# Kernel optimization log

Measured on AMD Instinct MI355X. Metric: run time of the kernel, lower is better.

Reference implementation:

```python
import jax, jax.numpy as jnp
import numpy as np

NUM_ITERATIONS = 3

def _squash(s):
    # Original squash reduces over the trailing singleton dim -> elementwise.
    sn = s * s
    return sn * s / ((1.0 + sn) * jnp.sqrt(sn))

def setup_inputs() -> dict:
    key = jax.random.key(0)
    k1, k2 = jax.random.split(key)
    x = jax.random.normal(k1, (128, 1152, 8), dtype=jnp.float32)
    W = jax.random.normal(k2, (1, 1152, 16, 16, 8), dtype=jnp.float32)
    return {"x": x, "W": W}

def reference(x, W):
    # x: [B, R, I]; W: [1, R, C, O, I]
    Wr = W[0]  # [R, C, O, I]
    # u_hat = W @ x broadcast over capsules: [B, R, C, O]
    u_hat = jnp.einsum('rcoi,bri->brco', Wr, x)
    R, C = Wr.shape[0], Wr.shape[1]
    b = jnp.zeros((R, C), dtype=x.dtype)  # routing logits (shared across batch)
    v = None
    for it in range(NUM_ITERATIONS):
        # legacy F.softmax on [1,R,C,1] -> dim=1 == routes axis
        c = jax.nn.softmax(b, axis=0)  # [R, C]
        s = jnp.einsum('rc,brco->bco', c, u_hat)  # [B, C, O]
        v = _squash(s)
        if it < NUM_ITERATIONS - 1:
            # agreement: <u_hat, v> averaged over batch
            a = jnp.einsum('brco,bco->brc', u_hat, v).mean(axis=0)  # [R, C]
            b = b + a
    return v  # [B, C, O] == v_j.squeeze(1).squeeze(-1)
```

## Files before the change

### kernel.cpp

```cpp
#include <hip/hip_runtime.h>
#include <math.h>

#define B_   128
#define R_   1152
#define C_   16
#define O_   16
#define RS_  64
#define RCH_ 18

#define WS_SP   0
#define WS_V    2097152
#define WS_BLOG 2129920
#define WS_WT   2148352

__device__ __forceinline__ float squashf(float s) {
    return s * fabsf(s) / (1.0f + s * s);
}

__global__ __launch_bounds__(512) void wtrans_k(const float* __restrict__ W,
                                                float* __restrict__ wt) {
    const int r = blockIdx.x;
    const int t = threadIdx.x;
    __shared__ float4 sh[520];
    const float4* __restrict__ W4 = (const float4*)W;
    float4* __restrict__ Wt4 = (float4*)wt;

    sh[(t & 7) * 65 + (t >> 3)] = W4[r * 512 + t];
    __syncthreads();
    Wt4[r * 512 + t] = sh[(t >> 6) * 65 + (t & 63)];
}

template <bool FIRST>
__global__ __launch_bounds__(256) void gemm_s_k(const float* __restrict__ x,
                                                const float* __restrict__ wt,
                                                const float* __restrict__ blog,
                                                float* __restrict__ sp) {
    const int bt  = blockIdx.x;
    const int rs  = blockIdx.y;
    const int t   = threadIdx.x;
    const int co4 = t & 63;
    const int b4  = t >> 6;
    const int c   = co4 >> 2;
    const int r0  = rs * RCH_;

    __shared__ float4 xl4[576];
    __shared__ float4 part[16];
    __shared__ float  colinv[16];
    __shared__ float  cwl[RCH_ * 16];

    const float4* __restrict__ X4  = (const float4*)x;
    const float4* __restrict__ Wt4 = (const float4*)wt;

    #pragma unroll
    for (int k = 0; k < 3; ++k) {
        const int u = t + k * 256;
        if (u < 576) {
            const int bl = u / 36, rem = u % 36;
            xl4[u] = X4[((bt * 16 + bl) * R_ + r0) * 2 + rem];
        }
    }

    if (!FIRST) {
        const float4* BL4 = (const float4*)blog;
        const int g = t & 3;
        float4 e4; e4.x = 0.f; e4.y = 0.f; e4.z = 0.f; e4.w = 0.f;
        #pragma unroll
        for (int i = 0; i < 18; ++i) {
            const float4 bv = BL4[i * 256 + t];
            e4.x += __expf(bv.x); e4.y += __expf(bv.y);
            e4.z += __expf(bv.z); e4.w += __expf(bv.w);
        }
        #pragma unroll
        for (int d = 4; d < 64; d <<= 1) {
            e4.x += __shfl_xor(e4.x, d); e4.y += __shfl_xor(e4.y, d);
            e4.z += __shfl_xor(e4.z, d); e4.w += __shfl_xor(e4.w, d);
        }
        if ((t & 63) < 4) part[(t >> 6) * 4 + g] = e4;
        __syncthreads();
        if (t < 4) {
            const float4 a = part[t], b = part[4 + t], cc4 = part[8 + t], d = part[12 + t];
            colinv[t * 4 + 0] = 1.0f / ((a.x + b.x) + (cc4.x + d.x));
            colinv[t * 4 + 1] = 1.0f / ((a.y + b.y) + (cc4.y + d.y));
            colinv[t * 4 + 2] = 1.0f / ((a.z + b.z) + (cc4.z + d.z));
            colinv[t * 4 + 3] = 1.0f / ((a.w + b.w) + (cc4.w + d.w));
        }
        __syncthreads();
        for (int u2 = t; u2 < RCH_ * 16; u2 += 256) {
            const int rl = u2 >> 4, cc = u2 & 15;
            cwl[u2] = __expf(blog[(r0 + rl) * 16 + cc]) * colinv[cc];
        }
    }
    __syncthreads();

    float acc[4][4];
    #pragma unroll
    for (int j = 0; j < 4; ++j)
        #pragma unroll
        for (int q = 0; q < 4; ++q) acc[j][q] = 0.f;

    #pragma unroll 3
    for (int rr = 0; rr < RCH_; ++rr) {
        const float cwv = FIRST ? (1.0f / (float)R_) : cwl[rr * 16 + c];
        const float4* wp = Wt4 + ((size_t)(r0 + rr) << 9) + co4;
        const float4 w0 = wp[  0], w1 = wp[ 64], w2 = wp[128], w3 = wp[192];
        const float4 w4 = wp[256], w5 = wp[320], w6 = wp[384], w7 = wp[448];
        #pragma unroll
        for (int j = 0; j < 4; ++j) {
            const float4 xa = xl4[(b4 * 4 + j) * 36 + rr * 2];
            const float4 xb = xl4[(b4 * 4 + j) * 36 + rr * 2 + 1];
            const float d0 = w0.x*xa.x + w0.y*xa.y + w0.z*xa.z + w0.w*xa.w
                           + w1.x*xb.x + w1.y*xb.y + w1.z*xb.z + w1.w*xb.w;
            const float d1 = w2.x*xa.x + w2.y*xa.y + w2.z*xa.z + w2.w*xa.w
                           + w3.x*xb.x + w3.y*xb.y + w3.z*xb.z + w3.w*xb.w;
            const float d2 = w4.x*xa.x + w4.y*xa.y + w4.z*xa.z + w4.w*xa.w
                           + w5.x*xb.x + w5.y*xb.y + w5.z*xb.z + w5.w*xb.w;
            const float d3 = w6.x*xa.x + w6.y*xa.y + w6.z*xa.z + w6.w*xa.w
                           + w7.x*xb.x + w7.y*xb.y + w7.z*xb.z + w7.w*xb.w;
            acc[j][0] = fmaf(cwv, d0, acc[j][0]);
            acc[j][1] = fmaf(cwv, d1, acc[j][1]);
            acc[j][2] = fmaf(cwv, d2, acc[j][2]);
            acc[j][3] = fmaf(cwv, d3, acc[j][3]);
        }
    }

    float4* sp4 = (float4*)sp;
    #pragma unroll
    for (int j = 0; j < 4; ++j) {
        const int b = bt * 16 + b4 * 4 + j;
        float4 o4; o4.x = acc[j][0]; o4.y = acc[j][1]; o4.z = acc[j][2]; o4.w = acc[j][3];
        sp4[(rs * B_ + b) * 64 + co4] = o4;
    }
}

__global__ __launch_bounds__(512) void reduce_squash_k(const float* __restrict__ sp,
                                                       float* __restrict__ outv) {
    const int t   = threadIdx.x;
    const int li  = t & 127;
    const int kq  = t >> 7;
    const int idx = blockIdx.x * 128 + li;
    const float* p = sp + (size_t)kq * 16 * 32768 + idx;
    float a0 = 0.f, a1 = 0.f, a2 = 0.f, a3 = 0.f;
    #pragma unroll
    for (int k = 0; k < 16; k += 4) {
        a0 += p[(k + 0) * 32768];
        a1 += p[(k + 1) * 32768];
        a2 += p[(k + 2) * 32768];
        a3 += p[(k + 3) * 32768];
    }
    __shared__ float red[512];
    red[t] = (a0 + a1) + (a2 + a3);
    __syncthreads();
    if (t < 128) {
        const float s = (red[t] + red[t + 128]) + (red[t + 256] + red[t + 384]);
        outv[idx] = squashf(s);
    }
}

template <bool FIRST>
__global__ __launch_bounds__(512) void a_k(const float* __restrict__ x,
                                           const float* __restrict__ wt,
                                           const float* __restrict__ v,
                                           float* __restrict__ blog) {
    const int r0 = blockIdx.x * 4;
    const int t  = threadIdx.x;
    const int w  = t >> 6, lane = t & 63;
    const int rr = w & 3, half = w >> 2;
    const int co4 = lane, c = lane >> 2;

    __shared__ float4 xl[128 * 8];
    __shared__ float  red[128];
    const float4* __restrict__ X4  = (const float4*)x;
    const float4* __restrict__ V4  = (const float4*)v;
    const float4* __restrict__ Wt4 = (const float4*)wt;

    #pragma unroll
    for (int kk = 0; kk < 2; ++kk) {
        const int u = t + kk * 512;
        const int b = u >> 3, rem = u & 7;
        xl[u] = X4[(b * R_ + r0) * 2 + rem];
    }
    __syncthreads();

    float y[8][4];
    #pragma unroll
    for (int i = 0; i < 8; ++i)
        #pragma unroll
        for (int q = 0; q < 4; ++q) y[i][q] = 0.f;

    const int b0 = half * 64;
    #pragma unroll 4
    for (int bb = 0; bb < 64; ++bb) {
        const int b = b0 + bb;
        const float4 xa = xl[b * 8 + rr * 2];
        const float4 xb = xl[b * 8 + rr * 2 + 1];
        const float4 vv = V4[b * 64 + co4];
        const float xs[8] = {xa.x, xa.y, xa.z, xa.w, xb.x, xb.y, xb.z, xb.w};
        #pragma unroll
        for (int i = 0; i < 8; ++i) {
            y[i][0] = fmaf(xs[i], vv.x, y[i][0]);
            y[i][1] = fmaf(xs[i], vv.y, y[i][1]);
            y[i][2] = fmaf(xs[i], vv.z, y[i][2]);
            y[i][3] = fmaf(xs[i], vv.w, y[i][3]);
        }
    }

    const float4* wp = Wt4 + ((size_t)(r0 + rr) << 9) + co4;
    float part = 0.f;
    #pragma unroll
    for (int q = 0; q < 4; ++q) {
        const float4 w0 = wp[(2 * q) * 64];
        const float4 w1 = wp[(2 * q + 1) * 64];
        part += w0.x*y[0][q] + w0.y*y[1][q] + w0.z*y[2][q] + w0.w*y[3][q]
              + w1.x*y[4][q] + w1.y*y[5][q] + w1.z*y[6][q] + w1.w*y[7][q];
    }
    part += __shfl_xor(part, 1);
    part += __shfl_xor(part, 2);
    if ((lane & 3) == 0) red[w * 16 + c] = part;
    __syncthreads();
    if (t < 64) {
        const int rr2 = t >> 4, cc = t & 15;
        const float val = (red[rr2 * 16 + cc] + red[(rr2 + 4) * 16 + cc]) * (1.0f / (float)B_);
        const int idx = (r0 + rr2) * 16 + cc;
        blog[idx] = FIRST ? val : (blog[idx] + val);
    }
}

extern "C" void kernel_launch(void* const* d_in, const int* in_sizes, int n_in,
                              void* d_out, int out_size, void* d_ws, size_t ws_size,
                              hipStream_t stream) {
    const float* x = (const float*)d_in[0];
    const float* W = (const float*)d_in[1];
    float* out = (float*)d_out;
    float* ws  = (float*)d_ws;

    float* sp   = ws + WS_SP;
    float* v    = ws + WS_V;
    float* blog = ws + WS_BLOG;
    float* wt   = ws + WS_WT;

    wtrans_k<<<R_, 512, 0, stream>>>(W, wt);

    gemm_s_k<true><<<dim3(8, RS_), 256, 0, stream>>>(x, wt, blog, sp);
    reduce_squash_k<<<256, 512, 0, stream>>>(sp, v);
    a_k<true><<<288, 512, 0, stream>>>(x, wt, v, blog);

    gemm_s_k<false><<<dim3(8, RS_), 256, 0, stream>>>(x, wt, blog, sp);
    reduce_squash_k<<<256, 512, 0, stream>>>(sp, v);
    a_k<false><<<288, 512, 0, stream>>>(x, wt, v, blog);

    gemm_s_k<false><<<dim3(8, RS_), 256, 0, stream>>>(x, wt, blog, sp);
    reduce_squash_k<<<256, 512, 0, stream>>>(sp, out);
}
```

Measured before the change: 179.3 us.

## Fuse reduce-squash into gemm via last-blocks finish, atomic softmax column sums

The separate reduce_squash kernel is removed. Each gemm block bumps an atomic counter, and the last 128 blocks spin until all blocks finish, then reduce the split-R partials and apply squash. The softmax column sums are now accumulated with atomics in the agreement kernel, so the gemm no longer recomputes them from the whole blog array. The kernel also adds register double-buffering of W loads, a block-index swizzle, and smaller agreement blocks. The spin-wait assumes all 512 blocks can be resident or finish, which risks a deadlock, and float atomics make the column sums nondeterministic.

Result: slower. 300.6 us (+67.7%).

```diff
diff --git a/kernel.cpp b/kernel.cpp
--- a/kernel.cpp
+++ b/kernel.cpp
@@ -7,24 +7,30 @@
 #define O_   16
 #define RS_  64
 #define RCH_ 18
+#define NBLK 512
+#define NFIN 128
 
 #define WS_SP   0
 #define WS_V    2097152
 #define WS_BLOG 2129920
-#define WS_WT   2148352
+#define WS_CTRL 2148352
+#define WS_WT   2148416
 
 __device__ __forceinline__ float squashf(float s) {
     return s * fabsf(s) / (1.0f + s * s);
 }
 
 __global__ __launch_bounds__(512) void wtrans_k(const float* __restrict__ W,
-                                                float* __restrict__ wt) {
+                                                float* __restrict__ wt,
+                                                float* __restrict__ ctrl) {
     const int r = blockIdx.x;
     const int t = threadIdx.x;
     __shared__ float4 sh[520];
     const float4* __restrict__ W4 = (const float4*)W;
     float4* __restrict__ Wt4 = (float4*)wt;
 
+    if (r == 0 && t < 64) ctrl[t] = 0.0f;
+
     sh[(t & 7) * 65 + (t >> 3)] = W4[r * 512 + t];
     __syncthreads();
     Wt4[r * 512 + t] = sh[(t >> 6) * 65 + (t & 63)];
@@ -34,9 +40,13 @@
 __global__ __launch_bounds__(256) void gemm_s_k(const float* __restrict__ x,
                                                 const float* __restrict__ wt,
                                                 const float* __restrict__ blog,
-                                                float* __restrict__ sp) {
-    const int bt  = blockIdx.x;
-    const int rs  = blockIdx.y;
+                                                const float* __restrict__ colsum,
+                                                float* __restrict__ sp,
+                                                float* __restrict__ dst,
+                                                unsigned int* __restrict__ ctr) {
+    const int bid = blockIdx.x;
+    const int bt  = bid >> 6;
+    const int rs  = ((bid & 7) << 3) | ((bid >> 3) & 7);
     const int t   = threadIdx.x;
     const int co4 = t & 63;
     const int b4  = t >> 6;
@@ -44,9 +54,10 @@
     const int r0  = rs * RCH_;
 
     __shared__ float4 xl4[576];
-    __shared__ float4 part[16];
-    __shared__ float  colinv[16];
     __shared__ float  cwl[RCH_ * 16];
+    __shared__ float  colinv_sh[16];
+    __shared__ float4 red[256];
+    __shared__ unsigned int old_sh;
 
     const float4* __restrict__ X4  = (const float4*)x;
     const float4* __restrict__ Wt4 = (const float4*)wt;
@@ -61,33 +72,11 @@
     }
 
     if (!FIRST) {
-        const float4* BL4 = (const float4*)blog;
-        const int g = t & 3;
-        float4 e4; e4.x = 0.f; e4.y = 0.f; e4.z = 0.f; e4.w = 0.f;
-        #pragma unroll
-        for (int i = 0; i < 18; ++i) {
-            const float4 bv = BL4[i * 256 + t];
-            e4.x += __expf(bv.x); e4.y += __expf(bv.y);
-            e4.z += __expf(bv.z); e4.w += __expf(bv.w);
-        }
-        #pragma unroll
-        for (int d = 4; d < 64; d <<= 1) {
-            e4.x += __shfl_xor(e4.x, d); e4.y += __shfl_xor(e4.y, d);
-            e4.z += __shfl_xor(e4.z, d); e4.w += __shfl_xor(e4.w, d);
-        }
-        if ((t & 63) < 4) part[(t >> 6) * 4 + g] = e4;
-        __syncthreads();
-        if (t < 4) {
-            const float4 a = part[t], b = part[4 + t], cc4 = part[8 + t], d = part[12 + t];
-            colinv[t * 4 + 0] = 1.0f / ((a.x + b.x) + (cc4.x + d.x));
-            colinv[t * 4 + 1] = 1.0f / ((a.y + b.y) + (cc4.y + d.y));
-            colinv[t * 4 + 2] = 1.0f / ((a.z + b.z) + (cc4.z + d.z));
-            colinv[t * 4 + 3] = 1.0f / ((a.w + b.w) + (cc4.w + d.w));
-        }
+        if (t < 16) colinv_sh[t] = 1.0f / colsum[t];
         __syncthreads();
         for (int u2 = t; u2 < RCH_ * 16; u2 += 256) {
             const int rl = u2 >> 4, cc = u2 & 15;
-            cwl[u2] = __expf(blog[(r0 + rl) * 16 + cc]) * colinv[cc];
+            cwl[u2] = __expf(blog[(r0 + rl) * 16 + cc]) * colinv_sh[cc];
         }
     }
     __syncthreads();
@@ -98,30 +87,43 @@
         #pragma unroll
         for (int q = 0; q < 4; ++q) acc[j][q] = 0.f;
 
-    #pragma unroll 3
-    for (int rr = 0; rr < RCH_; ++rr) {
+    const float4* __restrict__ wbase = Wt4 + ((size_t)r0 << 9) + co4;
+
+    auto body = [&](int rr, const float4* wv) {
         const float cwv = FIRST ? (1.0f / (float)R_) : cwl[rr * 16 + c];
-        const float4* wp = Wt4 + ((size_t)(r0 + rr) << 9) + co4;
-        const float4 w0 = wp[  0], w1 = wp[ 64], w2 = wp[128], w3 = wp[192];
-        const float4 w4 = wp[256], w5 = wp[320], w6 = wp[384], w7 = wp[448];
         #pragma unroll
         for (int j = 0; j < 4; ++j) {
             const float4 xa = xl4[(b4 * 4 + j) * 36 + rr * 2];
             const float4 xb = xl4[(b4 * 4 + j) * 36 + rr * 2 + 1];
-            const float d0 = w0.x*xa.x + w0.y*xa.y + w0.z*xa.z + w0.w*xa.w
-                           + w1.x*xb.x + w1.y*xb.y + w1.z*xb.z + w1.w*xb.w;
-            const float d1 = w2.x*xa.x + w2.y*xa.y + w2.z*xa.z + w2.w*xa.w
-                           + w3.x*xb.x + w3.y*xb.y + w3.z*xb.z + w3.w*xb.w;
-            const float d2 = w4.x*xa.x + w4.y*xa.y + w4.z*xa.z + w4.w*xa.w
-                           + w5.x*xb.x + w5.y*xb.y + w5.z*xb.z + w5.w*xb.w;
-            const float d3 = w6.x*xa.x + w6.y*xa.y + w6.z*xa.z + w6.w*xa.w
-                           + w7.x*xb.x + w7.y*xb.y + w7.z*xb.z + w7.w*xb.w;
+            const float d0 = wv[0].x*xa.x + wv[0].y*xa.y + wv[0].z*xa.z + wv[0].w*xa.w
+                           + wv[1].x*xb.x + wv[1].y*xb.y + wv[1].z*xb.z + wv[1].w*xb.w;
+            const float d1 = wv[2].x*xa.x + wv[2].y*xa.y + wv[2].z*xa.z + wv[2].w*xa.w
+                           + wv[3].x*xb.x + wv[3].y*xb.y + wv[3].z*xb.z + wv[3].w*xb.w;
+            const float d2 = wv[4].x*xa.x + wv[4].y*xa.y + wv[4].z*xa.z + wv[4].w*xa.w
+                           + wv[5].x*xb.x + wv[5].y*xb.y + wv[5].z*xb.z + wv[5].w*xb.w;
+            const float d3 = wv[6].x*xa.x + wv[6].y*xa.y + wv[6].z*xa.z + wv[6].w*xa.w
+                           + wv[7].x*xb.x + wv[7].y*xb.y + wv[7].z*xb.z + wv[7].w*xb.w;
             acc[j][0] = fmaf(cwv, d0, acc[j][0]);
             acc[j][1] = fmaf(cwv, d1, acc[j][1]);
             acc[j][2] = fmaf(cwv, d2, acc[j][2]);
             acc[j][3] = fmaf(cwv, d3, acc[j][3]);
         }
-    }
+    };
+
+    float4 w[8];
+    #pragma unroll
+    for (int q = 0; q < 8; ++q) w[q] = wbase[q * 64];
+    #pragma unroll 2
+    for (int rr = 0; rr < RCH_ - 1; ++rr) {
+        float4 wn[8];
+        const float4* wp = wbase + ((size_t)(rr + 1) << 9);
+        #pragma unroll
+        for (int q = 0; q < 8; ++q) wn[q] = wp[q * 64];
+        body(rr, w);
+        #pragma unroll
+        for (int q = 0; q < 8; ++q) w[q] = wn[q];
+    }
+    body(RCH_ - 1, w);
 
     float4* sp4 = (float4*)sp;
     #pragma unroll
@@ -130,53 +132,70 @@
         float4 o4; o4.x = acc[j][0]; o4.y = acc[j][1]; o4.z = acc[j][2]; o4.w = acc[j][3];
         sp4[(rs * B_ + b) * 64 + co4] = o4;
     }
-}
-
-__global__ __launch_bounds__(512) void reduce_squash_k(const float* __restrict__ sp,
-                                                       float* __restrict__ outv) {
-    const int t   = threadIdx.x;
-    const int li  = t & 127;
-    const int kq  = t >> 7;
-    const int idx = blockIdx.x * 128 + li;
-    const float* p = sp + (size_t)kq * 16 * 32768 + idx;
-    float a0 = 0.f, a1 = 0.f, a2 = 0.f, a3 = 0.f;
-    #pragma unroll
-    for (int k = 0; k < 16; k += 4) {
-        a0 += p[(k + 0) * 32768];
-        a1 += p[(k + 1) * 32768];
-        a2 += p[(k + 2) * 32768];
-        a3 += p[(k + 3) * 32768];
-    }
-    __shared__ float red[512];
-    red[t] = (a0 + a1) + (a2 + a3);
-    __syncthreads();
-    if (t < 128) {
-        const float s = (red[t] + red[t + 128]) + (red[t + 256] + red[t + 384]);
-        outv[idx] = squashf(s);
+
+    __syncthreads();
+    if (t == 0) {
+        __threadfence();
+        old_sh = atomicAdd(ctr, 1u);
+    }
+    __syncthreads();
+    const unsigned int old = old_sh;
+    if (old < (unsigned int)(NBLK - NFIN)) return;
+    const int fid = (int)old - (NBLK - NFIN);
+
+    if (t == 0) {
+        while (__hip_atomic_load(ctr, __ATOMIC_RELAXED, __HIP_MEMORY_SCOPE_AGENT)
+               < (unsigned int)NBLK) {
+            __builtin_amdgcn_s_sleep(2);
+        }
+    }
+    __syncthreads();
+    __threadfence();
+
+    const int li = t & 63, kq = t >> 6;
+    const int out4 = fid * 64 + li;
+    const float4* __restrict__ sp4c = (const float4*)sp;
+    float4 a; a.x = 0.f; a.y = 0.f; a.z = 0.f; a.w = 0.f;
+    #pragma unroll
+    for (int k = 0; k < 16; ++k) {
+        const float4 u = sp4c[(size_t)(kq * 16 + k) * 8192 + out4];
+        a.x += u.x; a.y += u.y; a.z += u.z; a.w += u.w;
+    }
+    red[t] = a;
+    __syncthreads();
+    if (t < 64) {
+        const float4 p0 = red[t], p1 = red[t + 64], p2 = red[t + 128], p3 = red[t + 192];
+        float4 o;
+        o.x = squashf((p0.x + p1.x) + (p2.x + p3.x));
+        o.y = squashf((p0.y + p1.y) + (p2.y + p3.y));
+        o.z = squashf((p0.z + p1.z) + (p2.z + p3.z));
+        o.w = squashf((p0.w + p1.w) + (p2.w + p3.w));
+        ((float4*)dst)[fid * 64 + t] = o;
     }
 }
 
 template <bool FIRST>
-__global__ __launch_bounds__(512) void a_k(const float* __restrict__ x,
+__global__ __launch_bounds__(256) void a_k(const float* __restrict__ x,
                                            const float* __restrict__ wt,
                                            const float* __restrict__ v,
-                                           float* __restrict__ blog) {
-    const int r0 = blockIdx.x * 4;
+                                           float* __restrict__ blog,
+                                           float* __restrict__ colsum) {
+    const int r0 = blockIdx.x * 2;
     const int t  = threadIdx.x;
     const int w  = t >> 6, lane = t & 63;
-    const int rr = w & 3, half = w >> 2;
+    const int rr = w & 1, half = w >> 1;
     const int co4 = lane, c = lane >> 2;
 
-    __shared__ float4 xl[128 * 8];
-    __shared__ float  red[128];
+    __shared__ float4 xl[128 * 4];
+    __shared__ float  red[64];
     const float4* __restrict__ X4  = (const float4*)x;
     const float4* __restrict__ V4  = (const float4*)v;
     const float4* __restrict__ Wt4 = (const float4*)wt;
 
     #pragma unroll
     for (int kk = 0; kk < 2; ++kk) {
-        const int u = t + kk * 512;
-        const int b = u >> 3, rem = u & 7;
+        const int u = t + kk * 256;
+        const int b = u >> 2, rem = u & 3;
         xl[u] = X4[(b * R_ + r0) * 2 + rem];
     }
     __syncthreads();
@@ -191,8 +210,8 @@
     #pragma unroll 4
     for (int bb = 0; bb < 64; ++bb) {
         const int b = b0 + bb;
-        const float4 xa = xl[b * 8 + rr * 2];
-        const float4 xb = xl[b * 8 + rr * 2 + 1];
+        const float4 xa = xl[b * 4 + rr * 2];
+        const float4 xb = xl[b * 4 + rr * 2 + 1];
         const float4 vv = V4[b * 64 + co4];
         const float xs[8] = {xa.x, xa.y, xa.z, xa.w, xb.x, xb.y, xb.z, xb.w};
         #pragma unroll
@@ -217,11 +236,13 @@
     part += __shfl_xor(part, 2);
     if ((lane & 3) == 0) red[w * 16 + c] = part;
     __syncthreads();
-    if (t < 64) {
+    if (t < 32) {
         const int rr2 = t >> 4, cc = t & 15;
-        const float val = (red[rr2 * 16 + cc] + red[(rr2 + 4) * 16 + cc]) * (1.0f / (float)B_);
+        const float val = (red[rr2 * 16 + cc] + red[(2 + rr2) * 16 + cc]) * (1.0f / (float)B_);
         const int idx = (r0 + rr2) * 16 + cc;
-        blog[idx] = FIRST ? val : (blog[idx] + val);
+        const float nv = FIRST ? val : (blog[idx] + val);
+        blog[idx] = nv;
+        atomicAdd(&colsum[cc], __expf(nv));
     }
 }
 
@@ -236,18 +257,20 @@
     float* sp   = ws + WS_SP;
     float* v    = ws + WS_V;
     float* blog = ws + WS_BLOG;
+    float* ctrl = ws + WS_CTRL;
     float* wt   = ws + WS_WT;
 
-    wtrans_k<<<R_, 512, 0, stream>>>(W, wt);
-
-    gemm_s_k<true><<<dim3(8, RS_), 256, 0, stream>>>(x, wt, blog, sp);
-    reduce_squash_k<<<256, 512, 0, stream>>>(sp, v);
-    a_k<true><<<288, 512, 0, stream>>>(x, wt, v, blog);
-
-    gemm_s_k<false><<<dim3(8, RS_), 256, 0, stream>>>(x, wt, blog, sp);
-    reduce_squash_k<<<256, 512, 0, stream>>>(sp, v);
-    a_k<false><<<288, 512, 0, stream>>>(x, wt, v, blog);
-
-    gemm_s_k<false><<<dim3(8, RS_), 256, 0, stream>>>(x, wt, blog, sp);
-    reduce_squash_k<<<256, 512, 0, stream>>>(sp, out);
-}
+    unsigned int* ctr = (unsigned int*)ctrl;
+    float* cs0 = ctrl + 16;
+    float* cs1 = ctrl + 32;
+
+    wtrans_k<<<R_, 512, 0, stream>>>(W, wt, ctrl);
+
+    gemm_s_k<true ><<<NBLK, 256, 0, stream>>>(x, wt, nullptr, nullptr, sp, v, ctr + 0);
+    a_k<true ><<<576, 256, 0, stream>>>(x, wt, v, blog, cs0);
+
+    gemm_s_k<false><<<NBLK, 256, 0, stream>>>(x, wt, blog, cs0, sp, v, ctr + 1);
+    a_k<false><<<576, 256, 0, stream>>>(x, wt, v, blog, cs1);
+
+    gemm_s_k<false><<<NBLK, 256, 0, stream>>>(x, wt, blog, cs1, sp, out, ctr + 2);
+}
```

## Fold softmax column sums into agreement kernel via atomics, remap gemm block order

Applied to the files above, without the earlier changes.

The agreement kernel now atomically accumulates exp of the updated routing logits into per-capsule column sums. Each gemm block then reads 16 precomputed sums instead of redundantly exponentiating and reducing the whole logit table. The gemm grid is also flattened to 1D, with a block-index swizzle that changes which route chunks run together, likely for cache locality on the shared weight slices. This adds float atomics with contention on 16 padded addresses, a nondeterministic summation order, and a control buffer that must be zeroed in the transpose kernel.

Result: slower. 225.6 us (+25.8%).

```diff
diff --git a/kernel.cpp b/kernel.cpp
--- a/kernel.cpp
+++ b/kernel.cpp
@@ -11,20 +11,26 @@
 #define WS_SP   0
 #define WS_V    2097152
 #define WS_BLOG 2129920
-#define WS_WT   2148352
+#define WS_CTRL 2148352
+#define WS_WT   2149120
 
 __device__ __forceinline__ float squashf(float s) {
     return s * fabsf(s) / (1.0f + s * s);
 }
 
 __global__ __launch_bounds__(512) void wtrans_k(const float* __restrict__ W,
-                                                float* __restrict__ wt) {
+                                                float* __restrict__ wt,
+                                                float* __restrict__ ctrl) {
     const int r = blockIdx.x;
     const int t = threadIdx.x;
     __shared__ float4 sh[520];
     const float4* __restrict__ W4 = (const float4*)W;
     float4* __restrict__ Wt4 = (float4*)wt;
 
+    if (r == 0) {
+        for (int u = t; u < 768; u += 512) ctrl[u] = 0.0f;
+    }
+
     sh[(t & 7) * 65 + (t >> 3)] = W4[r * 512 + t];
     __syncthreads();
     Wt4[r * 512 + t] = sh[(t >> 6) * 65 + (t & 63)];
@@ -34,9 +40,11 @@
 __global__ __launch_bounds__(256) void gemm_s_k(const float* __restrict__ x,
                                                 const float* __restrict__ wt,
                                                 const float* __restrict__ blog,
+                                                const float* __restrict__ colsum,
                                                 float* __restrict__ sp) {
-    const int bt  = blockIdx.x;
-    const int rs  = blockIdx.y;
+    const int bid = blockIdx.x;
+    const int rs  = (bid & 7) * 8 + ((bid >> 3) & 7);
+    const int bt  = bid >> 6;
     const int t   = threadIdx.x;
     const int co4 = t & 63;
     const int b4  = t >> 6;
@@ -44,9 +52,8 @@
     const int r0  = rs * RCH_;
 
     __shared__ float4 xl4[576];
-    __shared__ float4 part[16];
-    __shared__ float  colinv[16];
     __shared__ float  cwl[RCH_ * 16];
+    __shared__ float  colinv_sh[16];
 
     const float4* __restrict__ X4  = (const float4*)x;
     const float4* __restrict__ Wt4 = (const float4*)wt;
@@ -61,33 +68,11 @@
     }
 
     if (!FIRST) {
-        const float4* BL4 = (const float4*)blog;
-        const int g = t & 3;
-        float4 e4; e4.x = 0.f; e4.y = 0.f; e4.z = 0.f; e4.w = 0.f;
-        #pragma unroll
-        for (int i = 0; i < 18; ++i) {
-            const float4 bv = BL4[i * 256 + t];
-            e4.x += __expf(bv.x); e4.y += __expf(bv.y);
-            e4.z += __expf(bv.z); e4.w += __expf(bv.w);
-        }
-        #pragma unroll
-        for (int d = 4; d < 64; d <<= 1) {
-            e4.x += __shfl_xor(e4.x, d); e4.y += __shfl_xor(e4.y, d);
-            e4.z += __shfl_xor(e4.z, d); e4.w += __shfl_xor(e4.w, d);
-        }
-        if ((t & 63) < 4) part[(t >> 6) * 4 + g] = e4;
-        __syncthreads();
-        if (t < 4) {
-            const float4 a = part[t], b = part[4 + t], cc4 = part[8 + t], d = part[12 + t];
-            colinv[t * 4 + 0] = 1.0f / ((a.x + b.x) + (cc4.x + d.x));
-            colinv[t * 4 + 1] = 1.0f / ((a.y + b.y) + (cc4.y + d.y));
-            colinv[t * 4 + 2] = 1.0f / ((a.z + b.z) + (cc4.z + d.z));
-            colinv[t * 4 + 3] = 1.0f / ((a.w + b.w) + (cc4.w + d.w));
-        }
+        if (t < 16) colinv_sh[t] = 1.0f / colsum[t * 16];
         __syncthreads();
         for (int u2 = t; u2 < RCH_ * 16; u2 += 256) {
             const int rl = u2 >> 4, cc = u2 & 15;
-            cwl[u2] = __expf(blog[(r0 + rl) * 16 + cc]) * colinv[cc];
+            cwl[u2] = __expf(blog[(r0 + rl) * 16 + cc]) * colinv_sh[cc];
         }
     }
     __syncthreads();
@@ -160,7 +145,8 @@
 __global__ __launch_bounds__(512) void a_k(const float* __restrict__ x,
                                            const float* __restrict__ wt,
                                            const float* __restrict__ v,
-                                           float* __restrict__ blog) {
+                                           float* __restrict__ blog,
+                                           float* __restrict__ colsum) {
     const int r0 = blockIdx.x * 4;
     const int t  = threadIdx.x;
     const int w  = t >> 6, lane = t & 63;
@@ -221,7 +207,9 @@
         const int rr2 = t >> 4, cc = t & 15;
         const float val = (red[rr2 * 16 + cc] + red[(rr2 + 4) * 16 + cc]) * (1.0f / (float)B_);
         const int idx = (r0 + rr2) * 16 + cc;
-        blog[idx] = FIRST ? val : (blog[idx] + val);
+        const float nv = FIRST ? val : (blog[idx] + val);
+        blog[idx] = nv;
+        atomicAdd(&colsum[cc * 16], __expf(nv));
     }
 }
 
@@ -236,18 +224,22 @@
     float* sp   = ws + WS_SP;
     float* v    = ws + WS_V;
     float* blog = ws + WS_BLOG;
+    float* ctrl = ws + WS_CTRL;
     float* wt   = ws + WS_WT;
 
-    wtrans_k<<<R_, 512, 0, stream>>>(W, wt);
-
-    gemm_s_k<true><<<dim3(8, RS_), 256, 0, stream>>>(x, wt, blog, sp);
+    float* cs0 = ctrl + 256;
+    float* cs1 = ctrl + 512;
+
+    wtrans_k<<<R_, 512, 0, stream>>>(W, wt, ctrl);
+
+    gemm_s_k<true ><<<512, 256, 0, stream>>>(x, wt, nullptr, nullptr, sp);
     reduce_squash_k<<<256, 512, 0, stream>>>(sp, v);
-    a_k<true><<<288, 512, 0, stream>>>(x, wt, v, blog);
-
-    gemm_s_k<false><<<dim3(8, RS_), 256, 0, stream>>>(x, wt, blog, sp);
+    a_k<true ><<<288, 512, 0, stream>>>(x, wt, v, blog, cs0);
+
+    gemm_s_k<false><<<512, 256, 0, stream>>>(x, wt, blog, cs0, sp);
     reduce_squash_k<<<256, 512, 0, stream>>>(sp, v);
-    a_k<false><<<288, 512, 0, stream>>>(x, wt, v, blog);
-
-    gemm_s_k<false><<<dim3(8, RS_), 256, 0, stream>>>(x, wt, blog, sp);
+    a_k<false><<<288, 512, 0, stream>>>(x, wt, v, blog, cs1);
+
+    gemm_s_k<false><<<512, 256, 0, stream>>>(x, wt, blog, cs1, sp);
     reduce_squash_k<<<256, 512, 0, stream>>>(sp, out);
 }
```
